# Kernel tuning notes

Measured on AMD Instinct MI355X. Metric: run time of the kernel, lower is better.

Reference implementation:

```python
import jax, jax.numpy as jnp
import numpy as np

MC_SAMPLES = 32  # k neighbors
BIG = 1e8


def _swish(x):
    return x * jax.nn.sigmoid(x)


def setup_inputs() -> dict:
    key = jax.random.key(0)
    ks = jax.random.split(key, 8)
    bs, n, d, c = 8, 1024, 3, 64
    cmco_ci, hid = 16, 32
    abq_pairs = jax.random.normal(ks[0], (bs, n, n, d), dtype=jnp.float32)
    vals = jax.random.normal(ks[1], (bs, n, c), dtype=jnp.float32)
    mask = jnp.ones((bs, n), dtype=bool)
    s = 0.1
    return {
        "abq_pairs": abq_pairs,
        "vals": vals,
        "mask": mask,
        "W1": jax.random.normal(ks[2], (d, hid), dtype=jnp.float32) * s,
        "b1": jnp.zeros((hid,), jnp.float32),
        "W2": jax.random.normal(ks[3], (hid, hid), dtype=jnp.float32) * s,
        "b2": jnp.zeros((hid,), jnp.float32),
        "W3": jax.random.normal(ks[4], (hid, cmco_ci), dtype=jnp.float32) * s,
        "b3": jnp.zeros((cmco_ci,), jnp.float32),
        "Wl": jax.random.normal(ks[5], (c * cmco_ci, c), dtype=jnp.float32) * s,
        "bl": jnp.zeros((c,), jnp.float32),
    }


def reference(abq_pairs, vals, mask, W1, b1, W2, b2, W3, b3, Wl, bl):
    bs, n, _, d = abq_pairs.shape
    c = vals.shape[-1]
    k = min(MC_SAMPLES, n)

    # --- extract_neighborhood (knn branch, ds_frac=1 so queries = all points) ---
    # Trivial group distance = norm over last dim of abq pairs: (bs,n,n)
    dists = jnp.linalg.norm(abq_pairs, axis=-1)
    dists = jnp.where(mask[:, None, :], dists, BIG)
    _, nbhd_idx = jax.lax.top_k(-dists, k)  # smallest-k -> (bs, n, k)

    # gather neighbor pairwise embeddings: (bs, n, k, d)
    nbhd_abq = jnp.take_along_axis(abq_pairs, nbhd_idx[..., None], axis=2)
    # gather neighbor values and mask per batch: (bs, n, k, c), (bs, n, k)
    nbhd_vals = jax.vmap(lambda v, i: v[i])(vals, nbhd_idx)
    nbhd_mask = jax.vmap(lambda m, i: m[i])(mask, nbhd_idx) & mask[:, :, None]

    h = _swish(nbhd_abq @ W1 + b1)
    h = _swish(h @ W2 + b2)
    penult_kernel_weights = _swish(h @ W3 + b3)  # (bs, n, k, 16)

    # --- masked weighted aggregation (generalized PointConv trick) ---
    mW = jnp.where(nbhd_mask[..., None], penult_kernel_weights, 0.0)
    mV = jnp.where(nbhd_mask[..., None], nbhd_vals, 0.0)
    # vals^T @ weights -> (bs, n, c, 16) -> (bs, n, c*16)
    partial = jnp.einsum("bmkc,bmkp->bmcp", mV, mW).reshape(bs, n, -1)
    convolved = partial @ Wl + bl  # (bs, n, c)

    # zero out invalid query points
    return jnp.where(mask[..., None], convolved, 0.0)
```

## Files before the change

kernel.cpp:

```cpp
#include <hip/hip_runtime.h>
#include <math.h>


#define NPTS 1024
#define KNB  32
#define CCH  64
#define HID  32
#define PCH  16

__device__ __forceinline__ float swishf(float x) {
    return x / (1.0f + __expf(-x));
}

__global__ __launch_bounds__(256, 4) void lieconv_stage1(
    const float* __restrict__ abq, const float* __restrict__ vals,
    const float* __restrict__ W1, const float* __restrict__ b1,
    const float* __restrict__ W2, const float* __restrict__ b2,
    const float* __restrict__ W3, const float* __restrict__ b3,
    float* __restrict__ partial)
{
    __shared__ __align__(16) float s_buf[4][2048];
    __shared__ float s_nb[4][KNB][3];
    __shared__ int   s_sel[4][KNB];

    const int tid  = threadIdx.x;
    const int lane = tid & 63;
    const int w    = tid >> 6;
    const int row  = blockIdx.x * 4 + w;
    const int b    = row >> 10;
    const float* __restrict__ rowp = abq + (size_t)row * (NPTS * 3);

    float* sb = &s_buf[w][0];
    double* s_key    = (double*)sb;
    int*    s_cand_w = (int*)(sb + 128);

    float kf[16];
#pragma unroll
    for (int q = 0; q < 16; ++q) {
        int j = q * 64 + lane;
        float x = rowp[j * 3 + 0];
        float y = rowp[j * 3 + 1];
        float z = rowp[j * 3 + 2];
        kf[q] = fmaf(x, x, fmaf(y, y, z * z));
    }

    float kmax = kf[0];
#pragma unroll
    for (int q = 1; q < 16; ++q) kmax = fmaxf(kmax, kf[q]);
#pragma unroll
    for (int off = 32; off > 0; off >>= 1)
        kmax = fmaxf(kmax, __shfl_xor(kmax, off, 64));

    float lo = 0.0f, hi = kmax * 1.000001f + 1e-30f;
    float T  = hi;
    for (int it = 0; it < 28; ++it) {
        float mid = 0.5f * (lo + hi);
        int c = 0;
#pragma unroll
        for (int q = 0; q < 16; ++q)
            c += __popcll(__ballot(kf[q] < mid));
        if (c < KNB)      lo = mid;
        else if (c > 40)  hi = mid;
        else { T = mid; break; }
        T = hi;
    }
    float Tcut = T * 1.000001f;

    const unsigned long long lmask = (1ull << lane) - 1ull;
    int base = 0;
#pragma unroll
    for (int q = 0; q < 16; ++q) {
        bool p = kf[q] < Tcut;
        unsigned long long mk = __ballot(p);
        int pos = base + __popcll(mk & lmask);
        if (p && pos < 64) s_cand_w[pos] = q * 64 + lane;
        base += __popcll(mk);
    }
    int ncand = (base < 64) ? base : 64;
    __syncthreads();

    double ki; int ji;
    if (lane < ncand) {
        ji = s_cand_w[lane];
        double x = (double)rowp[ji * 3 + 0];
        double y = (double)rowp[ji * 3 + 1];
        double z = (double)rowp[ji * 3 + 2];
        ki = (x * x + y * y) + z * z;
    } else { ji = 0x7fffffff; ki = 1e300; }
    s_key[lane] = ki;
    __syncthreads();

    int rank = 0;
    for (int t = 0; t < ncand; ++t) {
        double kt = s_key[t];
        int    jt = s_cand_w[t];
        rank += (kt < ki || (kt == ki && jt < ji)) ? 1 : 0;
    }
    bool sel = (lane < ncand) && (rank < KNB);
    {
        unsigned long long mk = __ballot(sel);
        if (sel) s_sel[w][__popcll(mk & lmask)] = ji;
    }
    __syncthreads();

    if (lane < KNB) {
        int j = s_sel[w][lane];
        s_nb[w][lane][0] = rowp[j * 3 + 0];
        s_nb[w][lane][1] = rowp[j * 3 + 1];
        s_nb[w][lane][2] = rowp[j * 3 + 2];
    }
    const int o  = lane & 31;
    const int p  = lane & 15;
    float W1c[3], W2c[32], W3c[32];
#pragma unroll
    for (int e = 0; e < 3; ++e)  W1c[e] = W1[e * HID + o];
#pragma unroll
    for (int ii = 0; ii < 32; ++ii) W2c[ii] = W2[ii * HID + o];
#pragma unroll
    for (int ii = 0; ii < 32; ++ii) W3c[ii] = W3[ii * PCH + p];
    float b1o = b1[o], b2o = b2[o], b3p = b3[p];
    __syncthreads();

    float* bufA = sb;
    float* bufB = sb + 1024;

    {
        const int kh = lane >> 5;
#pragma unroll
        for (int pass = 0; pass < 16; ++pass) {
            int kk = pass * 2 + kh;
            float acc = b1o;
#pragma unroll
            for (int e = 0; e < 3; ++e) acc = fmaf(s_nb[w][kk][e], W1c[e], acc);
            bufA[kk * 32 + o] = swishf(acc);
        }
    }
    __syncthreads();

    {
        const int kh = lane >> 5;
#pragma unroll
        for (int pass = 0; pass < 16; ++pass) {
            int kk = pass * 2 + kh;
            float acc = b2o;
            const float4* hrow = (const float4*)&bufA[kk * 32];
#pragma unroll
            for (int i4 = 0; i4 < 8; ++i4) {
                float4 hv = hrow[i4];
                acc = fmaf(hv.x, W2c[i4 * 4 + 0], acc);
                acc = fmaf(hv.y, W2c[i4 * 4 + 1], acc);
                acc = fmaf(hv.z, W2c[i4 * 4 + 2], acc);
                acc = fmaf(hv.w, W2c[i4 * 4 + 3], acc);
            }
            bufB[kk * 32 + o] = swishf(acc);
        }
    }
    __syncthreads();

    float* s_w_w = sb;
    {
        const int k4 = lane >> 4;
#pragma unroll
        for (int pass = 0; pass < 8; ++pass) {
            int kk = pass * 4 + k4;
            float acc = b3p;
            const float4* hrow = (const float4*)&bufB[kk * 32];
#pragma unroll
            for (int i4 = 0; i4 < 8; ++i4) {
                float4 hv = hrow[i4];
                acc = fmaf(hv.x, W3c[i4 * 4 + 0], acc);
                acc = fmaf(hv.y, W3c[i4 * 4 + 1], acc);
                acc = fmaf(hv.z, W3c[i4 * 4 + 2], acc);
                acc = fmaf(hv.w, W3c[i4 * 4 + 3], acc);
            }
            s_w_w[kk * PCH + p] = swishf(acc);
        }
    }
    __syncthreads();

    const float* __restrict__ valsb = vals + (size_t)b * NPTS * CCH;
    float* chunk = sb + 1024;
    const int p4    = (lane & 3) * 4;
    const int cbase = lane >> 2;
    float acc[4][4];
#pragma unroll
    for (int it = 0; it < 4; ++it)
#pragma unroll
        for (int e = 0; e < 4; ++e) acc[it][e] = 0.0f;

    for (int ch = 0; ch < 2; ++ch) {
        __syncthreads();
#pragma unroll
        for (int kk2 = 0; kk2 < 16; ++kk2) {
            int j = s_sel[w][ch * 16 + kk2];
            chunk[kk2 * 64 + lane] = valsb[(size_t)j * CCH + lane];
        }
        __syncthreads();
#pragma unroll
        for (int kk2 = 0; kk2 < 16; ++kk2) {
            int kk = ch * 16 + kk2;
            float4 wv = *(const float4*)&s_w_w[kk * PCH + p4];
#pragma unroll
            for (int it = 0; it < 4; ++it) {
                float v = chunk[kk2 * 64 + cbase + 16 * it];
                acc[it][0] = fmaf(v, wv.x, acc[it][0]);
                acc[it][1] = fmaf(v, wv.y, acc[it][1]);
                acc[it][2] = fmaf(v, wv.z, acc[it][2]);
                acc[it][3] = fmaf(v, wv.w, acc[it][3]);
            }
        }
    }

    float* __restrict__ prow = partial + (size_t)row * (CCH * PCH);
#pragma unroll
    for (int it = 0; it < 4; ++it) {
        int c = cbase + 16 * it;
        float4 v = make_float4(acc[it][0], acc[it][1], acc[it][2], acc[it][3]);
        *(float4*)&prow[c * PCH + p4] = v;
    }
}

__global__ __launch_bounds__(256, 4) void lieconv_stage2(
    const float* __restrict__ partial, const float* __restrict__ Wl,
    const float* __restrict__ bl, float* __restrict__ out)
{
    __shared__ __align__(16) float s_part[8][1024];
    const int tid = threadIdx.x;
    const size_t r0 = (size_t)blockIdx.x * 8;

    const float4* gsrc = (const float4*)(partial + r0 * 1024);
    float4* ldst = (float4*)&s_part[0][0];
#pragma unroll
    for (int u = 0; u < 8; ++u) {
        int idx = u * 256 + tid;
        ldst[idx] = gsrc[idx];
    }
    __syncthreads();

    const int c  = tid & 63;
    const int rg = tid >> 6;
    float a0 = 0.0f, a1 = 0.0f;
    for (int k = 0; k < 1024; k += 4) {
        float4 q0 = *(const float4*)&s_part[rg][k];
        float4 q1 = *(const float4*)&s_part[rg + 4][k];
        float w0 = Wl[(size_t)(k + 0) * 64 + c];
        float w1 = Wl[(size_t)(k + 1) * 64 + c];
        float w2 = Wl[(size_t)(k + 2) * 64 + c];
        float w3 = Wl[(size_t)(k + 3) * 64 + c];
        a0 = fmaf(q0.x, w0, a0); a0 = fmaf(q0.y, w1, a0);
        a0 = fmaf(q0.z, w2, a0); a0 = fmaf(q0.w, w3, a0);
        a1 = fmaf(q1.x, w0, a1); a1 = fmaf(q1.y, w1, a1);
        a1 = fmaf(q1.z, w2, a1); a1 = fmaf(q1.w, w3, a1);
    }
    float bc = bl[c];
    out[(r0 + rg) * 64 + c]     = a0 + bc;
    out[(r0 + rg + 4) * 64 + c] = a1 + bc;
}

extern "C" void kernel_launch(void* const* d_in, const int* in_sizes, int n_in,
                              void* d_out, int out_size, void* d_ws, size_t ws_size,
                              hipStream_t stream)
{
    const float* abq  = (const float*)d_in[0];
    const float* vals = (const float*)d_in[1];
    const float* W1 = (const float*)d_in[3];
    const float* b1 = (const float*)d_in[4];
    const float* W2 = (const float*)d_in[5];
    const float* b2 = (const float*)d_in[6];
    const float* W3 = (const float*)d_in[7];
    const float* b3 = (const float*)d_in[8];
    const float* Wl = (const float*)d_in[9];
    const float* bl = (const float*)d_in[10];
    float* out = (float*)d_out;
    float* partial = (float*)d_ws;

    hipLaunchKernelGGL(lieconv_stage1, dim3(2048), dim3(256), 0, stream,
                       abq, vals, W1, b1, W2, b2, W3, b3, partial);
    hipLaunchKernelGGL(lieconv_stage2, dim3(1024), dim3(256), 0, stream,
                       partial, Wl, bl, out);
}
```

Before: 248.8 us.

## Split kNN selection and weight-net MLP into separate kernels with shuffle-based ranking

The fused stage-1 kernel becomes two kernels. A lightweight kNN kernel with a higher occupancy bound writes 16-bit neighbor indices into the output buffer as scratch. A 64-thread-per-row MLP/aggregation kernel then reads those indices. Candidate ranking now packs the double key and index into one 64-bit integer and compares via wavefront shuffles instead of shared memory and syncs. The aim is to let the memory-bound distance pass run at higher occupancy and drop block-wide syncs, at the cost of an extra launch and rereading abq rows for the neighbor coordinates.

```diff
diff --git a/kernel.cpp b/kernel.cpp
--- a/kernel.cpp
+++ b/kernel.cpp
@@ -12,27 +12,15 @@
     return x / (1.0f + __expf(-x));
 }
 
-__global__ __launch_bounds__(256, 4) void lieconv_stage1(
-    const float* __restrict__ abq, const float* __restrict__ vals,
-    const float* __restrict__ W1, const float* __restrict__ b1,
-    const float* __restrict__ W2, const float* __restrict__ b2,
-    const float* __restrict__ W3, const float* __restrict__ b3,
-    float* __restrict__ partial)
-{
-    __shared__ __align__(16) float s_buf[4][2048];
-    __shared__ float s_nb[4][KNB][3];
-    __shared__ int   s_sel[4][KNB];
-
+__global__ __launch_bounds__(256, 8) void lieconv_knn(
+    const float* __restrict__ abq, unsigned short* __restrict__ sel_out)
+{
+    __shared__ int s_cand[4][64];
     const int tid  = threadIdx.x;
     const int lane = tid & 63;
     const int w    = tid >> 6;
     const int row  = blockIdx.x * 4 + w;
-    const int b    = row >> 10;
     const float* __restrict__ rowp = abq + (size_t)row * (NPTS * 3);
-
-    float* sb = &s_buf[w][0];
-    double* s_key    = (double*)sb;
-    int*    s_cand_w = (int*)(sb + 128);
 
     float kf[16];
 #pragma unroll
@@ -43,7 +31,6 @@
         float z = rowp[j * 3 + 2];
         kf[q] = fmaf(x, x, fmaf(y, y, z * z));
     }
-
     float kmax = kf[0];
 #pragma unroll
     for (int q = 1; q < 16; ++q) kmax = fmaxf(kmax, kf[q]);
@@ -51,8 +38,7 @@
     for (int off = 32; off > 0; off >>= 1)
         kmax = fmaxf(kmax, __shfl_xor(kmax, off, 64));
 
-    float lo = 0.0f, hi = kmax * 1.000001f + 1e-30f;
-    float T  = hi;
+    float lo = 0.0f, hi = kmax * 1.000001f + 1e-30f, T = hi;
     for (int it = 0; it < 28; ++it) {
         float mid = 0.5f * (lo + hi);
         int c = 0;
@@ -73,44 +59,58 @@
         bool p = kf[q] < Tcut;
         unsigned long long mk = __ballot(p);
         int pos = base + __popcll(mk & lmask);
-        if (p && pos < 64) s_cand_w[pos] = q * 64 + lane;
+        if (p && pos < 64) s_cand[w][pos] = q * 64 + lane;
         base += __popcll(mk);
     }
     int ncand = (base < 64) ? base : 64;
-    __syncthreads();
-
-    double ki; int ji;
+
+    unsigned long long ci = ~0ull;
+    int ji = 0x7fffffff;
     if (lane < ncand) {
-        ji = s_cand_w[lane];
+        ji = s_cand[w][lane];
         double x = (double)rowp[ji * 3 + 0];
         double y = (double)rowp[ji * 3 + 1];
         double z = (double)rowp[ji * 3 + 2];
-        ki = (x * x + y * y) + z * z;
-    } else { ji = 0x7fffffff; ki = 1e300; }
-    s_key[lane] = ki;
-    __syncthreads();
-
+        double ki = (x * x + y * y) + z * z;
+        ci = ((unsigned long long)__double_as_longlong(ki) & ~1023ull) | (unsigned)ji;
+    }
     int rank = 0;
-    for (int t = 0; t < ncand; ++t) {
-        double kt = s_key[t];
-        int    jt = s_cand_w[t];
-        rank += (kt < ki || (kt == ki && jt < ji)) ? 1 : 0;
+#pragma unroll
+    for (int t = 0; t < 64; ++t) {
+        unsigned long long ct = __shfl(ci, t, 64);
+        rank += (ct < ci) ? 1 : 0;
     }
     bool sel = (lane < ncand) && (rank < KNB);
-    {
-        unsigned long long mk = __ballot(sel);
-        if (sel) s_sel[w][__popcll(mk & lmask)] = ji;
-    }
-    __syncthreads();
+    unsigned long long mk = __ballot(sel);
+    if (sel) sel_out[(size_t)row * KNB + __popcll(mk & lmask)] = (unsigned short)ji;
+}
+
+__global__ __launch_bounds__(64, 4) void lieconv_mlp(
+    const float* __restrict__ abq, const float* __restrict__ vals,
+    const unsigned short* __restrict__ sel_in,
+    const float* __restrict__ W1, const float* __restrict__ b1,
+    const float* __restrict__ W2, const float* __restrict__ b2,
+    const float* __restrict__ W3, const float* __restrict__ b3,
+    float* __restrict__ partial)
+{
+    __shared__ __align__(16) float s_buf[2048];
+    __shared__ float s_nb[KNB][3];
+    __shared__ int   s_sel[KNB];
+
+    const int lane = threadIdx.x;
+    const int row  = blockIdx.x;
+    const int b    = row >> 10;
+    const float* __restrict__ rowp = abq + (size_t)row * (NPTS * 3);
 
     if (lane < KNB) {
-        int j = s_sel[w][lane];
-        s_nb[w][lane][0] = rowp[j * 3 + 0];
-        s_nb[w][lane][1] = rowp[j * 3 + 1];
-        s_nb[w][lane][2] = rowp[j * 3 + 2];
-    }
-    const int o  = lane & 31;
-    const int p  = lane & 15;
+        int j = (int)sel_in[(size_t)row * KNB + lane];
+        s_sel[lane] = j;
+        s_nb[lane][0] = rowp[j * 3 + 0];
+        s_nb[lane][1] = rowp[j * 3 + 1];
+        s_nb[lane][2] = rowp[j * 3 + 2];
+    }
+    const int o = lane & 31;
+    const int p = lane & 15;
     float W1c[3], W2c[32], W3c[32];
 #pragma unroll
     for (int e = 0; e < 3; ++e)  W1c[e] = W1[e * HID + o];
@@ -121,8 +121,8 @@
     float b1o = b1[o], b2o = b2[o], b3p = b3[p];
     __syncthreads();
 
-    float* bufA = sb;
-    float* bufB = sb + 1024;
+    float* bufA = s_buf;
+    float* bufB = s_buf + 1024;
 
     {
         const int kh = lane >> 5;
@@ -131,7 +131,7 @@
             int kk = pass * 2 + kh;
             float acc = b1o;
 #pragma unroll
-            for (int e = 0; e < 3; ++e) acc = fmaf(s_nb[w][kk][e], W1c[e], acc);
+            for (int e = 0; e < 3; ++e) acc = fmaf(s_nb[kk][e], W1c[e], acc);
             bufA[kk * 32 + o] = swishf(acc);
         }
     }
@@ -157,7 +157,7 @@
     }
     __syncthreads();
 
-    float* s_w_w = sb;
+    float* s_w = s_buf;
     {
         const int k4 = lane >> 4;
 #pragma unroll
@@ -173,13 +173,13 @@
                 acc = fmaf(hv.z, W3c[i4 * 4 + 2], acc);
                 acc = fmaf(hv.w, W3c[i4 * 4 + 3], acc);
             }
-            s_w_w[kk * PCH + p] = swishf(acc);
+            s_w[kk * PCH + p] = swishf(acc);
         }
     }
     __syncthreads();
 
     const float* __restrict__ valsb = vals + (size_t)b * NPTS * CCH;
-    float* chunk = sb + 1024;
+    float* chunk = s_buf + 1024;
     const int p4    = (lane & 3) * 4;
     const int cbase = lane >> 2;
     float acc[4][4];
@@ -192,14 +192,14 @@
         __syncthreads();
 #pragma unroll
         for (int kk2 = 0; kk2 < 16; ++kk2) {
-            int j = s_sel[w][ch * 16 + kk2];
+            int j = s_sel[ch * 16 + kk2];
             chunk[kk2 * 64 + lane] = valsb[(size_t)j * CCH + lane];
         }
         __syncthreads();
 #pragma unroll
         for (int kk2 = 0; kk2 < 16; ++kk2) {
             int kk = ch * 16 + kk2;
-            float4 wv = *(const float4*)&s_w_w[kk * PCH + p4];
+            float4 wv = *(const float4*)&s_w[kk * PCH + p4];
 #pragma unroll
             for (int it = 0; it < 4; ++it) {
                 float v = chunk[kk2 * 64 + cbase + 16 * it];
@@ -273,9 +273,11 @@
     const float* bl = (const float*)d_in[10];
     float* out = (float*)d_out;
     float* partial = (float*)d_ws;
-
-    hipLaunchKernelGGL(lieconv_stage1, dim3(2048), dim3(256), 0, stream,
-                       abq, vals, W1, b1, W2, b2, W3, b3, partial);
+    unsigned short* sel = (unsigned short*)d_out;
+
+    hipLaunchKernelGGL(lieconv_knn, dim3(2048), dim3(256), 0, stream, abq, sel);
+    hipLaunchKernelGGL(lieconv_mlp, dim3(8192), dim3(64), 0, stream,
+                       abq, vals, sel, W1, b1, W2, b2, W3, b3, partial);
     hipLaunchKernelGGL(lieconv_stage2, dim3(1024), dim3(256), 0, stream,
                        partial, Wl, bl, out);
 }
```

After: 247.4 us. Within noise of the previous version (-0.5%).
